# Kernel tuning notes

Measured on AMD Instinct MI355X. Metric: run time of the kernel, lower is better.

## Reference

```python
import jax, jax.numpy as jnp
import numpy as np

N_NODES = 50000


def gcn_conv(x, W, b, src, dst, n):
    # PyG GCNConv: linear transform, add self-loops, symmetric normalization,
    # scatter-add aggregation from src -> dst, then bias.
    h = x @ W  # [N, out]
    loop = jnp.arange(n, dtype=src.dtype)
    s = jnp.concatenate([src, loop])
    d = jnp.concatenate([dst, loop])
    deg = jax.ops.segment_sum(jnp.ones(s.shape[0], dtype=h.dtype), d, num_segments=n)
    dinv = jnp.where(deg > 0, jax.lax.rsqrt(deg), 0.0)
    norm = dinv[s] * dinv[d]  # [E+N]
    msg = h[s] * norm[:, None]
    out = jax.ops.segment_sum(msg, d, num_segments=n)
    return out + b


def setup_inputs() -> dict:
    key = jax.random.key(0)
    ks = jax.random.split(key, 10)
    F_in, H, C = 256, 128, 128
    E, EL = 320000, 200000
    x = jax.random.normal(ks[0], (N_NODES, F_in), dtype=jnp.float32)
    edge_index = jax.random.randint(ks[1], (2, E), 0, N_NODES, dtype=jnp.int32)
    edge_label_index = jax.random.randint(ks[2], (2, EL), 0, N_NODES, dtype=jnp.int32)
    def glorot(k, shape):
        lim = np.sqrt(6.0 / (shape[0] + shape[1]))
        return jax.random.uniform(k, shape, jnp.float32, -lim, lim)
    W0 = glorot(ks[3], (F_in, H))
    b0 = jnp.zeros((H,), jnp.float32)
    W1 = glorot(ks[4], (H, H))
    b1 = jnp.zeros((H,), jnp.float32)
    W2 = glorot(ks[5], (H, C))
    b2 = jnp.zeros((C,), jnp.float32)
    return {"x": x, "edge_index": edge_index, "edge_label_index": edge_label_index,
            "W0": W0, "b0": b0, "W1": W1, "b1": b1, "W2": W2, "b2": b2}


def reference(x, edge_index, edge_label_index, W0, b0, W1, b1, W2, b2):
    src, dst = edge_index[0], edge_index[1]
    n = x.shape[0]
    # drop_edge keep_ratio == 1.0 -> all edges kept (deterministic)
    h = jax.nn.relu(gcn_conv(x, W0, b0, src, dst, n))
    h = jax.nn.relu(gcn_conv(h, W1, b1, src, dst, n))
    z = gcn_conv(h, W2, b2, src, dst, n)  # final conv, no activation
    # decode: dot product over candidate edge pairs
    eli = edge_label_index.astype(jnp.int32)
    logits = jnp.sum(z[eli[0]] * z[eli[1]], axis=-1)  # [E_label]
    return logits
```

## Files before the change

### kernel.cpp

```cpp
#include <hip/hip_runtime.h>
#include <hip/hip_bf16.h>


typedef __attribute__((ext_vector_type(8))) short short8v;
typedef __attribute__((ext_vector_type(4))) float f32x4;

__device__ inline unsigned bf16_rne(float f) {
    unsigned u = __float_as_uint(f);
    return (u + 0x7FFF + ((u >> 16) & 1)) >> 16;
}


__device__ inline void split_pack_one(const float* W, short* Whp, short* Wlp,
                                      int idx, int K) {
    int k = idx >> 7, col = idx & 127;
    float f = W[idx];
    unsigned h = bf16_rne(f);
    float fh = __uint_as_float(h << 16);
    unsigned l = bf16_rne(f - fh);
    int NS = K >> 5;
    int c = col >> 4, col16 = col & 15, s = k >> 5, q = (k >> 3) & 3, j = k & 7;
    int waddr = (c * NS + s) * 512 + q * 128 + col16 * 8 + j;
    Whp[waddr] = (short)h;
    Wlp[waddr] = (short)l;
}

__global__ __launch_bounds__(256) void preamble_kernel(
        const float* __restrict__ W0, short* __restrict__ W0h, short* __restrict__ W0l,
        const float* __restrict__ W1, short* __restrict__ W1h, short* __restrict__ W1l,
        const float* __restrict__ W2, short* __restrict__ W2h, short* __restrict__ W2l,
        const float* __restrict__ x, short* __restrict__ Axp,
        int* __restrict__ off, int* __restrict__ fill,
        int n, int F_in, int H, int ntiles, int total) {
    int gid = blockIdx.x * blockDim.x + threadIdx.x;
    if (gid >= total) return;
    int idx = gid;
    if (idx < n) { off[idx] = 0; fill[idx] = 0; return; }
    idx -= n;
    int n0 = F_in * H, n12 = H * H;
    if (idx < n0) { split_pack_one(W0, W0h, W0l, idx, F_in); return; }
    idx -= n0;
    if (idx < n12) { split_pack_one(W1, W1h, W1l, idx, H); return; }
    idx -= n12;
    if (idx < n12) { split_pack_one(W2, W2h, W2l, idx, H); return; }
    idx -= n12;
    const int K = F_in;
    const int CH = K / 8;
    int r  = idx & 15;
    int c8 = (idx >> 4) % CH;
    int g  = idx / (16 * CH);
    int row = g * 16 + r;
    if (row >= n) row = n - 1;
    const float* xp = x + (size_t)row * K + c8 * 8;
    float4 v0 = *reinterpret_cast<const float4*>(xp);
    float4 v1 = *reinterpret_cast<const float4*>(xp + 4);
    float f[8] = {v0.x, v0.y, v0.z, v0.w, v1.x, v1.y, v1.z, v1.w};
    short8v hv, lv;
#pragma unroll
    for (int j = 0; j < 8; ++j) {
        unsigned h = bf16_rne(f[j]);
        float fh = __uint_as_float(h << 16);
        unsigned l = bf16_rne(f[j] - fh);
        hv[j] = (short)h;
        lv[j] = (short)l;
    }
    size_t base = (size_t)g * (16 * K * 2) + c8 * 128 + r * 8;
    *reinterpret_cast<short8v*>(&Axp[base]) = hv;
    *reinterpret_cast<short8v*>(&Axp[base + 16 * K]) = lv;
}


__global__ void count_deg_kernel(const int* __restrict__ dst, int* __restrict__ deg, int E) {
    int e = blockIdx.x * blockDim.x + threadIdx.x;
    if (e < E) atomicAdd(&deg[dst[e]], 1);
}

__global__ __launch_bounds__(1024) void scan1_kernel(int* __restrict__ data,
                                                     int* __restrict__ sums, int n) {
    __shared__ int tmp[1024];
    int t = threadIdx.x;
    int idx = blockIdx.x * 1024 + t;
    int val = (idx < n) ? data[idx] : 0;
    tmp[t] = val;
    __syncthreads();
#pragma unroll
    for (int off = 1; off < 1024; off <<= 1) {
        int v = (t >= off) ? tmp[t - off] : 0;
        __syncthreads();
        tmp[t] += v;
        __syncthreads();
    }
    if (idx < n) data[idx] = tmp[t] - val;
    if (t == 1023) sums[blockIdx.x] = tmp[t];
}

__global__ void scan2_kernel(int* __restrict__ sums, int nb) {
    int lane = threadIdx.x & 63;
    int v = (lane < nb) ? sums[lane] : 0;
    int orig = v;
#pragma unroll
    for (int d = 1; d < 64; d <<= 1) {
        int t2 = __shfl_up(v, d, 64);
        if (lane >= d) v += t2;
    }
    if (lane < nb) sums[lane] = v - orig;
}

__global__ __launch_bounds__(1024) void scan3_kernel(int* __restrict__ data,
                                                     const int* __restrict__ sums, int n) {
    int idx = blockIdx.x * 1024 + threadIdx.x;
    if (idx < n && blockIdx.x > 0) data[idx] += sums[blockIdx.x];
}

__global__ void make_dinv_kernel(const int* __restrict__ off, float* __restrict__ dinv,
                                 int n, int E) {
    int v = blockIdx.x * blockDim.x + threadIdx.x;
    if (v < n) {
        int o1 = (v + 1 < n) ? off[v + 1] : E;
        float d = (float)(o1 - off[v]) + 1.0f;
        dinv[v] = 1.0f / sqrtf(d);
    }
}

__global__ void csr_fill_kernel(const int* __restrict__ src, const int* __restrict__ dst,
                                const int* __restrict__ off, int* __restrict__ fill,
                                int* __restrict__ csr_src, int E) {
    int e = blockIdx.x * blockDim.x + threadIdx.x;
    if (e >= E) return;
    int d = dst[e];
    int pos = atomicAdd(&fill[d], 1);
    csr_src[off[d] + pos] = src[e];
}


template<int K>
__global__ __launch_bounds__(256) void gemm_mfma_packed(const short* __restrict__ Axp,
                                                        const short* __restrict__ Whp,
                                                        const short* __restrict__ Wlp,
                                                        const float* __restrict__ dinv,
                                                        float* __restrict__ out,
                                                        int M) {
    constexpr int NS = K / 32;
    constexpr size_t TILE = (size_t)16 * K * 2;
    const int lane = threadIdx.x & 63;
    const int w = threadIdx.x >> 6;
    const int gtile = blockIdx.x * 2 + (w >> 1);
    const int chalf = (w & 1) * 4;
    const int row16 = gtile * 16;
    if (row16 >= M) return;

    const short* ab = Axp + (size_t)gtile * TILE + lane * 8;
    const short* lb = ab + 16 * K;

    short8v ah[NS], al[NS];
#pragma unroll
    for (int s = 0; s < NS; ++s) {
        ah[s] = *reinterpret_cast<const short8v*>(ab + s * 512);
        al[s] = *reinterpret_cast<const short8v*>(lb + s * 512);
    }

    f32x4 acc[4];
#pragma unroll
    for (int c = 0; c < 4; ++c) acc[c] = (f32x4){0.f, 0.f, 0.f, 0.f};

#pragma unroll
    for (int c4 = 0; c4 < 4; ++c4) {
        int c = chalf + c4;
        const short* bb = Whp + (size_t)(c * NS) * 512 + lane * 8;
        const short* cb = Wlp + (size_t)(c * NS) * 512 + lane * 8;
#pragma unroll
        for (int s = 0; s < NS; ++s) {
            short8v bh = *reinterpret_cast<const short8v*>(bb + s * 512);
            short8v bl = *reinterpret_cast<const short8v*>(cb + s * 512);
            acc[c4] = __builtin_amdgcn_mfma_f32_16x16x32_bf16(ah[s], bh, acc[c4], 0, 0, 0);
            acc[c4] = __builtin_amdgcn_mfma_f32_16x16x32_bf16(ah[s], bl, acc[c4], 0, 0, 0);
            acc[c4] = __builtin_amdgcn_mfma_f32_16x16x32_bf16(al[s], bh, acc[c4], 0, 0, 0);
        }
    }

#pragma unroll
    for (int r = 0; r < 4; ++r) {
        int row = row16 + (lane >> 4) * 4 + r;
        if (row < M) {
            float ds = dinv[row];
#pragma unroll
            for (int c4 = 0; c4 < 4; ++c4)
                out[(size_t)row * 128 + (chalf + c4) * 16 + (lane & 15)] = acc[c4][r] * ds;
        }
    }
}


template<int PACKED>
__global__ __launch_bounds__(1024) void gather_kernel(const int* __restrict__ off,
                                                      const int* __restrict__ csr_src,
                                                      const float* __restrict__ dinv,
                                                      const float* __restrict__ hp,
                                                      const float* __restrict__ bias,
                                                      float* __restrict__ outf,
                                                      short* __restrict__ Axp,
                                                      int n, int E, int do_relu) {
    int v = blockIdx.x * 16 + (threadIdx.x >> 6);
    int lane = threadIdx.x & 63;
    if (v >= n) return;

    int o0 = off[v];
    int o1 = (v + 1 < n) ? off[v + 1] : E;

    const float2* __restrict__ hp2 = reinterpret_cast<const float2*>(hp);
    float2 sv = hp2[(size_t)v * 64 + lane];
    float ax = sv.x, ay = sv.y;
    float bx = 0.0f, by = 0.0f;

    for (int base = o0; base < o1; base += 64) {
        int cnt = min(64, o1 - base);
        int myidx = (lane < cnt) ? csr_src[base + lane] : 0;
        int j = 0;
        for (; j + 8 <= cnt; j += 8) {
            int i0 = __shfl(myidx, j,     64);
            int i1 = __shfl(myidx, j + 1, 64);
            int i2 = __shfl(myidx, j + 2, 64);
            int i3 = __shfl(myidx, j + 3, 64);
            int i4 = __shfl(myidx, j + 4, 64);
            int i5 = __shfl(myidx, j + 5, 64);
            int i6 = __shfl(myidx, j + 6, 64);
            int i7 = __shfl(myidx, j + 7, 64);
            float2 h0 = hp2[(size_t)i0 * 64 + lane];
            float2 h1 = hp2[(size_t)i1 * 64 + lane];
            float2 h2 = hp2[(size_t)i2 * 64 + lane];
            float2 h3 = hp2[(size_t)i3 * 64 + lane];
            float2 h4 = hp2[(size_t)i4 * 64 + lane];
            float2 h5 = hp2[(size_t)i5 * 64 + lane];
            float2 h6 = hp2[(size_t)i6 * 64 + lane];
            float2 h7 = hp2[(size_t)i7 * 64 + lane];
            ax += h0.x; ay += h0.y;  bx += h1.x; by += h1.y;
            ax += h2.x; ay += h2.y;  bx += h3.x; by += h3.y;
            ax += h4.x; ay += h4.y;  bx += h5.x; by += h5.y;
            ax += h6.x; ay += h6.y;  bx += h7.x; by += h7.y;
        }
        for (; j + 4 <= cnt; j += 4) {
            int i0 = __shfl(myidx, j,     64);
            int i1 = __shfl(myidx, j + 1, 64);
            int i2 = __shfl(myidx, j + 2, 64);
            int i3 = __shfl(myidx, j + 3, 64);
            float2 h0 = hp2[(size_t)i0 * 64 + lane];
            float2 h1 = hp2[(size_t)i1 * 64 + lane];
            float2 h2 = hp2[(size_t)i2 * 64 + lane];
            float2 h3 = hp2[(size_t)i3 * 64 + lane];
            ax += h0.x; ay += h0.y;  bx += h1.x; by += h1.y;
            ax += h2.x; ay += h2.y;  bx += h3.x; by += h3.y;
        }
        for (; j < cnt; ++j) {
            int s = __shfl(myidx, j, 64);
            float2 hv = hp2[(size_t)s * 64 + lane];
            ax += hv.x; ay += hv.y;
        }
    }

    float dv = dinv[v];
    float2 bb = *reinterpret_cast<const float2*>(&bias[lane * 2]);
    float ox = dv * (ax + bx) + bb.x;
    float oy = dv * (ay + by) + bb.y;
    if (do_relu) { ox = fmaxf(ox, 0.0f); oy = fmaxf(oy, 0.0f); }

    if (PACKED) {
        unsigned h0 = bf16_rne(ox);
        unsigned l0 = bf16_rne(ox - __uint_as_float(h0 << 16));
        unsigned h1 = bf16_rne(oy);
        unsigned l1 = bf16_rne(oy - __uint_as_float(h1 << 16));
        int g = v >> 4, r = v & 15;
        size_t a = (size_t)g * 4096 + (lane >> 2) * 128 + r * 8 + ((2 * lane) & 7);
        *reinterpret_cast<short2*>(&Axp[a])        = make_short2((short)h0, (short)h1);
        *reinterpret_cast<short2*>(&Axp[a + 2048]) = make_short2((short)l0, (short)l1);
    } else {
        *reinterpret_cast<float2*>(&outf[(size_t)v * 128 + lane * 2]) = make_float2(ox, oy);
    }
}


__global__ __launch_bounds__(256) void decode_kernel(const int* __restrict__ ia,
                                                     const int* __restrict__ ib,
                                                     const float* __restrict__ z,
                                                     float* __restrict__ out, int EL) {
    int gid = blockIdx.x * blockDim.x + threadIdx.x;
    int e = gid >> 5;
    int l5 = gid & 31;
    if (e >= EL) return;
    int a = ia[e], b = ib[e];
    const float4* z4 = reinterpret_cast<const float4*>(z);
    float4 za = z4[(size_t)a * 32 + l5];
    float4 zb = z4[(size_t)b * 32 + l5];
    float s = za.x * zb.x + za.y * zb.y + za.z * zb.z + za.w * zb.w;
#pragma unroll
    for (int off = 16; off > 0; off >>= 1) s += __shfl_down(s, off, 64);
    if (l5 == 0) out[e] = s;
}


extern "C" void kernel_launch(void* const* d_in, const int* in_sizes, int n_in,
                              void* d_out, int out_size, void* d_ws, size_t ws_size,
                              hipStream_t stream) {
    const float* x   = (const float*)d_in[0];
    const int*   ei  = (const int*)d_in[1];
    const int*   eli = (const int*)d_in[2];
    const float* W0  = (const float*)d_in[3];
    const float* b0  = (const float*)d_in[4];
    const float* W1  = (const float*)d_in[5];
    const float* b1  = (const float*)d_in[6];
    const float* W2  = (const float*)d_in[7];
    const float* b2  = (const float*)d_in[8];
    float* out = (float*)d_out;

    const int H    = in_sizes[4];
    const int F_in = in_sizes[3] / H;
    const int n    = in_sizes[0] / F_in;
    const int E    = in_sizes[1] / 2;
    const int EL   = in_sizes[2] / 2;

    const int* src = ei;
    const int* dst = ei + E;
    const int* la  = eli;
    const int* lb  = eli + EL;

    const int ntiles = (n + 15) / 16;

    char* ws = (char*)d_ws;
    size_t p = 0;
    auto alloc = [&](size_t bytes) { char* r = ws + p; p = (p + bytes + 255) & ~(size_t)255; return r; };
    float* dinv    = (float*)alloc((size_t)n * 4);
    int*   off     = (int*)  alloc((size_t)n * 4);
    int*   csr_src = (int*)  alloc((size_t)E * 4);
    int*   sums    = (int*)  alloc(64 * 4);
    short* W0h     = (short*)alloc((size_t)F_in * H * 2);
    short* W0l     = (short*)alloc((size_t)F_in * H * 2);
    short* W1h     = (short*)alloc((size_t)H * H * 2);
    short* W1l     = (short*)alloc((size_t)H * H * 2);
    short* W2h     = (short*)alloc((size_t)H * H * 2);
    short* W2l     = (short*)alloc((size_t)H * H * 2);
    short* Axp     = (short*)alloc((size_t)ntiles * 16 * F_in * 2 * 2);
    float* bufA    = (float*)alloc((size_t)n * 128 * 4);
    float* bufB    = (float*)alloc((size_t)n * 128 * 4);
    int*   fill    = (int*)bufB;

    const int T = 256;
    dim3 blk(T);

    {
        int n0 = F_in * H, n12 = H * H;
        long long total = (long long)n + n0 + 2 * n12 + (long long)ntiles * 16 * (F_in / 8);
        preamble_kernel<<<(int)((total + T - 1) / T), blk, 0, stream>>>(
            W0, W0h, W0l, W1, W1h, W1l, W2, W2h, W2l, x, Axp, off, fill,
            n, F_in, H, ntiles, (int)total);
    }
    count_deg_kernel<<<(E + T - 1) / T, blk, 0, stream>>>(dst, off, E);
    int nb = (n + 1023) / 1024;
    scan1_kernel<<<nb, 1024, 0, stream>>>(off, sums, n);
    scan2_kernel<<<1, 64, 0, stream>>>(sums, nb);
    scan3_kernel<<<nb, 1024, 0, stream>>>(off, sums, n);
    make_dinv_kernel<<<(n + T - 1) / T, blk, 0, stream>>>(off, dinv, n, E);
    csr_fill_kernel<<<(E + T - 1) / T, blk, 0, stream>>>(src, dst, off, fill, csr_src, E);

    const int mblocks       = (ntiles + 1) / 2;
    const int gather_blocks = (n + 15) / 16;

    gemm_mfma_packed<256><<<mblocks, blk, 0, stream>>>(Axp, W0h, W0l, dinv, bufA, n);
    gather_kernel<1><<<gather_blocks, 1024, 0, stream>>>(off, csr_src, dinv, bufA, b0,
                                                         nullptr, Axp, n, E, 1);

    gemm_mfma_packed<128><<<mblocks, blk, 0, stream>>>(Axp, W1h, W1l, dinv, bufA, n);
    gather_kernel<1><<<gather_blocks, 1024, 0, stream>>>(off, csr_src, dinv, bufA, b1,
                                                         nullptr, Axp, n, E, 1);

    gemm_mfma_packed<128><<<mblocks, blk, 0, stream>>>(Axp, W2h, W2l, dinv, bufA, n);
    gather_kernel<0><<<gather_blocks, 1024, 0, stream>>>(off, csr_src, dinv, bufA, b2,
                                                         bufB, nullptr, n, E, 0);

    const int dec_blocks = (int)(((long long)EL * 32 + T - 1) / T);
    decode_kernel<<<dec_blocks, blk, 0, stream>>>(la, lb, bufB, out, EL);
}
```

Before: 331.8 us.

## Drop dinv and scan2 kernels, recompute dinv inline, use half-wave float4 gather

Removes the scan2 and make_dinv launches: scan3 blocks sum earlier block totals themselves, and the inverse square-root degree is recomputed from CSR offsets in the gemm epilogue and the gather. The gather now assigns 32 lanes per node with float4 loads, so each wave handles two nodes and the Axp writes are wider. This reduces launch overhead and idle lanes on low-degree nodes, at the cost of a smaller unroll and some redundant offset reads.

```diff
diff --git a/kernel.cpp b/kernel.cpp
--- a/kernel.cpp
+++ b/kernel.cpp
@@ -3,6 +3,7 @@
 
 
 typedef __attribute__((ext_vector_type(8))) short short8v;
+typedef __attribute__((ext_vector_type(4))) short short4v;
 typedef __attribute__((ext_vector_type(4))) float f32x4;
 
 __device__ inline unsigned bf16_rne(float f) {
@@ -94,32 +95,17 @@
     if (t == 1023) sums[blockIdx.x] = tmp[t];
 }
 
-__global__ void scan2_kernel(int* __restrict__ sums, int nb) {
-    int lane = threadIdx.x & 63;
-    int v = (lane < nb) ? sums[lane] : 0;
-    int orig = v;
-#pragma unroll
-    for (int d = 1; d < 64; d <<= 1) {
-        int t2 = __shfl_up(v, d, 64);
-        if (lane >= d) v += t2;
-    }
-    if (lane < nb) sums[lane] = v - orig;
-}
-
 __global__ __launch_bounds__(1024) void scan3_kernel(int* __restrict__ data,
                                                      const int* __restrict__ sums, int n) {
+    __shared__ int base;
+    if (threadIdx.x == 0) {
+        int s = 0;
+        for (int b = 0; b < blockIdx.x; ++b) s += sums[b];
+        base = s;
+    }
+    __syncthreads();
     int idx = blockIdx.x * 1024 + threadIdx.x;
-    if (idx < n && blockIdx.x > 0) data[idx] += sums[blockIdx.x];
-}
-
-__global__ void make_dinv_kernel(const int* __restrict__ off, float* __restrict__ dinv,
-                                 int n, int E) {
-    int v = blockIdx.x * blockDim.x + threadIdx.x;
-    if (v < n) {
-        int o1 = (v + 1 < n) ? off[v + 1] : E;
-        float d = (float)(o1 - off[v]) + 1.0f;
-        dinv[v] = 1.0f / sqrtf(d);
-    }
+    if (idx < n && blockIdx.x > 0) data[idx] += base;
 }
 
 __global__ void csr_fill_kernel(const int* __restrict__ src, const int* __restrict__ dst,
@@ -137,9 +123,9 @@
 __global__ __launch_bounds__(256) void gemm_mfma_packed(const short* __restrict__ Axp,
                                                         const short* __restrict__ Whp,
                                                         const short* __restrict__ Wlp,
-                                                        const float* __restrict__ dinv,
+                                                        const int* __restrict__ off,
                                                         float* __restrict__ out,
-                                                        int M) {
+                                                        int M, int E) {
     constexpr int NS = K / 32;
     constexpr size_t TILE = (size_t)16 * K * 2;
     const int lane = threadIdx.x & 63;
@@ -182,7 +168,9 @@
     for (int r = 0; r < 4; ++r) {
         int row = row16 + (lane >> 4) * 4 + r;
         if (row < M) {
-            float ds = dinv[row];
+            int o0 = off[row];
+            int o1 = (row + 1 < M) ? off[row + 1] : E;
+            float ds = 1.0f / sqrtf((float)(o1 - o0) + 1.0f);
 #pragma unroll
             for (int c4 = 0; c4 < 4; ++c4)
                 out[(size_t)row * 128 + (chalf + c4) * 16 + (lane & 15)] = acc[c4][r] * ds;
@@ -194,86 +182,77 @@
 template<int PACKED>
 __global__ __launch_bounds__(1024) void gather_kernel(const int* __restrict__ off,
                                                       const int* __restrict__ csr_src,
-                                                      const float* __restrict__ dinv,
                                                       const float* __restrict__ hp,
                                                       const float* __restrict__ bias,
                                                       float* __restrict__ outf,
                                                       short* __restrict__ Axp,
                                                       int n, int E, int do_relu) {
-    int v = blockIdx.x * 16 + (threadIdx.x >> 6);
-    int lane = threadIdx.x & 63;
+    int v = blockIdx.x * 32 + (threadIdx.x >> 5);
+    int l5 = threadIdx.x & 31;
     if (v >= n) return;
 
     int o0 = off[v];
     int o1 = (v + 1 < n) ? off[v + 1] : E;
-
-    const float2* __restrict__ hp2 = reinterpret_cast<const float2*>(hp);
-    float2 sv = hp2[(size_t)v * 64 + lane];
-    float ax = sv.x, ay = sv.y;
-    float bx = 0.0f, by = 0.0f;
-
-    for (int base = o0; base < o1; base += 64) {
-        int cnt = min(64, o1 - base);
-        int myidx = (lane < cnt) ? csr_src[base + lane] : 0;
+    float dv = 1.0f / sqrtf((float)(o1 - o0) + 1.0f);
+
+    const float4* __restrict__ hp4 = reinterpret_cast<const float4*>(hp);
+    float4 sv = hp4[(size_t)v * 32 + l5];
+    float ax = sv.x, ay = sv.y, az = sv.z, aw = sv.w;
+    float bx = 0.f, by = 0.f, bz = 0.f, bw = 0.f;
+
+    for (int base = o0; base < o1; base += 32) {
+        int cnt = min(32, o1 - base);
+        int myidx = (l5 < cnt) ? csr_src[base + l5] : 0;
         int j = 0;
-        for (; j + 8 <= cnt; j += 8) {
-            int i0 = __shfl(myidx, j,     64);
-            int i1 = __shfl(myidx, j + 1, 64);
-            int i2 = __shfl(myidx, j + 2, 64);
-            int i3 = __shfl(myidx, j + 3, 64);
-            int i4 = __shfl(myidx, j + 4, 64);
-            int i5 = __shfl(myidx, j + 5, 64);
-            int i6 = __shfl(myidx, j + 6, 64);
-            int i7 = __shfl(myidx, j + 7, 64);
-            float2 h0 = hp2[(size_t)i0 * 64 + lane];
-            float2 h1 = hp2[(size_t)i1 * 64 + lane];
-            float2 h2 = hp2[(size_t)i2 * 64 + lane];
-            float2 h3 = hp2[(size_t)i3 * 64 + lane];
-            float2 h4 = hp2[(size_t)i4 * 64 + lane];
-            float2 h5 = hp2[(size_t)i5 * 64 + lane];
-            float2 h6 = hp2[(size_t)i6 * 64 + lane];
-            float2 h7 = hp2[(size_t)i7 * 64 + lane];
-            ax += h0.x; ay += h0.y;  bx += h1.x; by += h1.y;
-            ax += h2.x; ay += h2.y;  bx += h3.x; by += h3.y;
-            ax += h4.x; ay += h4.y;  bx += h5.x; by += h5.y;
-            ax += h6.x; ay += h6.y;  bx += h7.x; by += h7.y;
-        }
         for (; j + 4 <= cnt; j += 4) {
-            int i0 = __shfl(myidx, j,     64);
-            int i1 = __shfl(myidx, j + 1, 64);
-            int i2 = __shfl(myidx, j + 2, 64);
-            int i3 = __shfl(myidx, j + 3, 64);
-            float2 h0 = hp2[(size_t)i0 * 64 + lane];
-            float2 h1 = hp2[(size_t)i1 * 64 + lane];
-            float2 h2 = hp2[(size_t)i2 * 64 + lane];
-            float2 h3 = hp2[(size_t)i3 * 64 + lane];
-            ax += h0.x; ay += h0.y;  bx += h1.x; by += h1.y;
-            ax += h2.x; ay += h2.y;  bx += h3.x; by += h3.y;
+            int i0 = __shfl(myidx, j,     32);
+            int i1 = __shfl(myidx, j + 1, 32);
+            int i2 = __shfl(myidx, j + 2, 32);
+            int i3 = __shfl(myidx, j + 3, 32);
+            float4 h0 = hp4[(size_t)i0 * 32 + l5];
+            float4 h1 = hp4[(size_t)i1 * 32 + l5];
+            float4 h2 = hp4[(size_t)i2 * 32 + l5];
+            float4 h3 = hp4[(size_t)i3 * 32 + l5];
+            ax += h0.x; ay += h0.y; az += h0.z; aw += h0.w;
+            bx += h1.x; by += h1.y; bz += h1.z; bw += h1.w;
+            ax += h2.x; ay += h2.y; az += h2.z; aw += h2.w;
+            bx += h3.x; by += h3.y; bz += h3.z; bw += h3.w;
         }
         for (; j < cnt; ++j) {
-            int s = __shfl(myidx, j, 64);
-            float2 hv = hp2[(size_t)s * 64 + lane];
-            ax += hv.x; ay += hv.y;
-        }
-    }
-
-    float dv = dinv[v];
-    float2 bb = *reinterpret_cast<const float2*>(&bias[lane * 2]);
+            int s = __shfl(myidx, j, 32);
+            float4 hv = hp4[(size_t)s * 32 + l5];
+            ax += hv.x; ay += hv.y; az += hv.z; aw += hv.w;
+        }
+    }
+
+    float4 bb = reinterpret_cast<const float4*>(bias)[l5];
     float ox = dv * (ax + bx) + bb.x;
     float oy = dv * (ay + by) + bb.y;
-    if (do_relu) { ox = fmaxf(ox, 0.0f); oy = fmaxf(oy, 0.0f); }
+    float oz = dv * (az + bz) + bb.z;
+    float ow = dv * (aw + bw) + bb.w;
+    if (do_relu) {
+        ox = fmaxf(ox, 0.0f); oy = fmaxf(oy, 0.0f);
+        oz = fmaxf(oz, 0.0f); ow = fmaxf(ow, 0.0f);
+    }
 
     if (PACKED) {
-        unsigned h0 = bf16_rne(ox);
-        unsigned l0 = bf16_rne(ox - __uint_as_float(h0 << 16));
-        unsigned h1 = bf16_rne(oy);
-        unsigned l1 = bf16_rne(oy - __uint_as_float(h1 << 16));
+        float f[4] = {ox, oy, oz, ow};
+        short4v hv, lv;
+#pragma unroll
+        for (int j = 0; j < 4; ++j) {
+            unsigned h = bf16_rne(f[j]);
+            float fh = __uint_as_float(h << 16);
+            unsigned l = bf16_rne(f[j] - fh);
+            hv[j] = (short)h;
+            lv[j] = (short)l;
+        }
         int g = v >> 4, r = v & 15;
-        size_t a = (size_t)g * 4096 + (lane >> 2) * 128 + r * 8 + ((2 * lane) & 7);
-        *reinterpret_cast<short2*>(&Axp[a])        = make_short2((short)h0, (short)h1);
-        *reinterpret_cast<short2*>(&Axp[a + 2048]) = make_short2((short)l0, (short)l1);
+        size_t a = (size_t)g * 4096 + (l5 >> 1) * 128 + r * 8 + (l5 & 1) * 4;
+        *reinterpret_cast<short4v*>(&Axp[a])        = hv;
+        *reinterpret_cast<short4v*>(&Axp[a + 2048]) = lv;
     } else {
-        *reinterpret_cast<float2*>(&outf[(size_t)v * 128 + lane * 2]) = make_float2(ox, oy);
+        float4 ov = make_float4(ox, oy, oz, ow);
+        reinterpret_cast<float4*>(outf)[(size_t)v * 32 + l5] = ov;
     }
 }
 
@@ -327,7 +306,6 @@
     char* ws = (char*)d_ws;
     size_t p = 0;
     auto alloc = [&](size_t bytes) { char* r = ws + p; p = (p + bytes + 255) & ~(size_t)255; return r; };
-    float* dinv    = (float*)alloc((size_t)n * 4);
     int*   off     = (int*)  alloc((size_t)n * 4);
     int*   csr_src = (int*)  alloc((size_t)E * 4);
     int*   sums    = (int*)  alloc(64 * 4);
@@ -355,24 +333,22 @@
     count_deg_kernel<<<(E + T - 1) / T, blk, 0, stream>>>(dst, off, E);
     int nb = (n + 1023) / 1024;
     scan1_kernel<<<nb, 1024, 0, stream>>>(off, sums, n);
-    scan2_kernel<<<1, 64, 0, stream>>>(sums, nb);
     scan3_kernel<<<nb, 1024, 0, stream>>>(off, sums, n);
-    make_dinv_kernel<<<(n + T - 1) / T, blk, 0, stream>>>(off, dinv, n, E);
     csr_fill_kernel<<<(E + T - 1) / T, blk, 0, stream>>>(src, dst, off, fill, csr_src, E);
 
     const int mblocks       = (ntiles + 1) / 2;
-    const int gather_blocks = (n + 15) / 16;
-
-    gemm_mfma_packed<256><<<mblocks, blk, 0, stream>>>(Axp, W0h, W0l, dinv, bufA, n);
-    gather_kernel<1><<<gather_blocks, 1024, 0, stream>>>(off, csr_src, dinv, bufA, b0,
+    const int gather_blocks = (n + 31) / 32;
+
+    gemm_mfma_packed<256><<<mblocks, blk, 0, stream>>>(Axp, W0h, W0l, off, bufA, n, E);
+    gather_kernel<1><<<gather_blocks, 1024, 0, stream>>>(off, csr_src, bufA, b0,
                                                          nullptr, Axp, n, E, 1);
 
-    gemm_mfma_packed<128><<<mblocks, blk, 0, stream>>>(Axp, W1h, W1l, dinv, bufA, n);
-    gather_kernel<1><<<gather_blocks, 1024, 0, stream>>>(off, csr_src, dinv, bufA, b1,
+    gemm_mfma_packed<128><<<mblocks, blk, 0, stream>>>(Axp, W1h, W1l, off, bufA, n, E);
+    gather_kernel<1><<<gather_blocks, 1024, 0, stream>>>(off, csr_src, bufA, b1,
                                                          nullptr, Axp, n, E, 1);
 
-    gemm_mfma_packed<128><<<mblocks, blk, 0, stream>>>(Axp, W2h, W2l, dinv, bufA, n);
-    gather_kernel<0><<<gather_blocks, 1024, 0, stream>>>(off, csr_src, dinv, bufA, b2,
+    gemm_mfma_packed<128><<<mblocks, blk, 0, stream>>>(Axp, W2h, W2l, off, bufA, n, E);
+    gather_kernel<0><<<gather_blocks, 1024, 0, stream>>>(off, csr_src, bufA, b2,
                                                          bufB, nullptr, n, E, 0);
 
     const int dec_blocks = (int)(((long long)EL * 32 + T - 1) / T);
```

After: 322.1 us. 2.9% less time.
